# Optimization experiments

Measured on AMD Instinct MI355X. Metric: run time of the kernel, lower is better.

Reference implementation:

```python
import jax, jax.numpy as jnp
import numpy as np

N_HEADS = 16
HEAD_SIZE = 64

def setup_inputs() -> dict:
    key = jax.random.key(0)
    k1, k2 = jax.random.split(key)
    B, N, D = 2, 2048, N_HEADS * HEAD_SIZE
    x = jax.random.normal(k1, (B, N, D), dtype=jnp.float32)
    # lecun_normal-ish scale for the QKV kernel
    W_qkv = jax.random.normal(k2, (D, 3 * D), dtype=jnp.float32) * (1.0 / np.sqrt(D))
    return {"x": x, "W_qkv": W_qkv}

def reference(x, W_qkv):
    B, N, D = x.shape
    H, Dh = N_HEADS, HEAD_SIZE
    qkv = x @ W_qkv                                  # [B,N,3D]
    q, k, v = jnp.split(qkv, 3, axis=-1)
    q = q.reshape(B, N, H, Dh)
    k = k.reshape(B, N, H, Dh)
    v = v.reshape(B, N, H, Dh)
    dist = jnp.einsum('bihd,bjhd->bhij', q, k) / jnp.sqrt(jnp.asarray(Dh, dtype=x.dtype))
    mask = jnp.tril(jnp.ones((N, N), dtype=bool))[None, None, :, :]
    dist = jnp.where(mask, dist, -jnp.inf)
    attn = jax.nn.softmax(dist, axis=-1)             # [B,H,N,N]
    out_heads = jnp.einsum('bhij,bjhd->bihd', attn, v)
    return out_heads.reshape(B, N, H * Dh)
```

## Files before the change

kernel.cpp:

```cpp
#include <hip/hip_runtime.h>

typedef __attribute__((ext_vector_type(8))) short bf16x8;
typedef __attribute__((ext_vector_type(4))) float f32x4;
typedef __attribute__((ext_vector_type(16))) float f32x16;
typedef __attribute__((ext_vector_type(2))) unsigned int u32x2;

#define DEVI static __device__ __forceinline__

namespace {
constexpr int NSEQ = 2048, NH = 16;
constexpr int D = 1024, D3 = 3072;
}

DEVI unsigned short f2bf(float f) {
  union { float f; unsigned int u; } v; v.f = f;
  unsigned int r = v.u + 0x7FFFu + ((v.u >> 16) & 1u);
  return (unsigned short)(r >> 16);
}

DEVI void gload16(const unsigned short* g, unsigned short* lds_) {
  __builtin_amdgcn_global_load_lds(
      (const __attribute__((address_space(1))) unsigned int*)g,
      (__attribute__((address_space(3))) unsigned int*)lds_, 16, 0, 0);
}

DEVI f32x4 mfma16(bf16x8 a, bf16x8 b, f32x4 c) {
  return __builtin_amdgcn_mfma_f32_16x16x32_bf16(a, b, c, 0, 0, 0);
}

DEVI f32x16 mfma32(bf16x8 a, bf16x8 b, f32x16 c) {
  return __builtin_amdgcn_mfma_f32_32x32x16_bf16(a, b, c, 0, 0, 0);
}

DEVI float exp2g(float x) {
#if __has_builtin(__builtin_amdgcn_exp2f)
  return __builtin_amdgcn_exp2f(x);
#else
  return exp2f(x);
#endif
}

DEVI unsigned int cvtpk(float a, float b) {
  unsigned int r;
  asm("v_cvt_pk_bf16_f32 %0, %1, %2" : "=v"(r) : "v"(a), "v"(b));
  return r;
}

DEVI u32x2 pswap2(unsigned int a, unsigned int b) {
  return __builtin_amdgcn_permlane32_swap(a, b, false, false);
}
DEVI float xmax_halves(float v) {
  union { float f; unsigned int u; } c; c.f = v;
  u32x2 r = pswap2(c.u, c.u);
  union { unsigned int u; float f; } x, y; x.u = r.x; y.u = r.y;
  return fmaxf(x.f, y.f);
}

union U4 { unsigned int u[4]; bf16x8 v; };

__global__ __launch_bounds__(256) void prep_k(const float* __restrict__ x,
                                              const float* __restrict__ W,
                                              unsigned short* __restrict__ xb,
                                              unsigned short* __restrict__ Wt) {
  __shared__ float t[32][33];
  const int bid = blockIdx.x;
  if (bid < 4096) {
    int i = (bid * 256 + threadIdx.x) * 4;
    float4 v = *reinterpret_cast<const float4*>(x + i);
    ushort4 o;
    o.x = f2bf(v.x); o.y = f2bf(v.y); o.z = f2bf(v.z); o.w = f2bf(v.w);
    *reinterpret_cast<ushort4*>(xb + i) = o;
  } else {
    const int b2 = bid - 4096;
    const int c0 = (b2 % 96) * 32, k0 = (b2 / 96) * 32;
    const int tx = threadIdx.x & 31, ty = threadIdx.x >> 5;
#pragma unroll
    for (int r = 0; r < 32; r += 8)
      t[ty + r][tx] = W[(size_t)(k0 + ty + r) * D3 + c0 + tx];
    __syncthreads();
#pragma unroll
    for (int r = 0; r < 32; r += 8)
      Wt[(size_t)(c0 + ty + r) * D + k0 + tx] = f2bf(t[tx][ty + r]);
  }
}

__global__ __launch_bounds__(256) void qkv_gemm_k(const unsigned short* __restrict__ xb,
                                                  const unsigned short* __restrict__ Wt,
                                                  unsigned short* __restrict__ qw,
                                                  unsigned short* __restrict__ kw,
                                                  unsigned short* __restrict__ vtw) {
  __shared__ unsigned short smA[128 * 32];
  __shared__ unsigned short smB[128 * 32];
  const int tid = threadIdx.x, w = tid >> 6, l = tid & 63;
  const int m0 = blockIdx.x * 128, n0 = blockIdx.y * 128;
  const int wm = w >> 1, wn = w & 1;

  const unsigned short* ga[2]; const unsigned short* gb[2];
  unsigned short* la[2]; unsigned short* lb[2];
#pragma unroll
  for (int i = 0; i < 2; ++i) {
    int idx = tid + i * 256;
    int row = idx >> 2;
    int blk = (idx & 3) ^ ((row >> 1) & 3);
    ga[i] = xb + (size_t)(m0 + row) * D + blk * 8;
    gb[i] = Wt + (size_t)(n0 + row) * D + blk * 8;
    la[i] = smA + (w * 64 + i * 256) * 8;
    lb[i] = smB + (w * 64 + i * 256) * 8;
  }

  f32x4 acc[4][4];
#pragma unroll
  for (int a = 0; a < 4; ++a)
#pragma unroll
    for (int b = 0; b < 4; ++b) acc[a][b] = (f32x4){0.f, 0.f, 0.f, 0.f};

  for (int kt = 0; kt < D / 32; ++kt) {
    __syncthreads();
#pragma unroll
    for (int i = 0; i < 2; ++i) {
      gload16(ga[i] + kt * 32, la[i]);
      gload16(gb[i] + kt * 32, lb[i]);
    }
    asm volatile("s_waitcnt vmcnt(0)" ::: "memory");
    __syncthreads();

    bf16x8 af[4], bfr[4];
#pragma unroll
    for (int a = 0; a < 4; ++a) {
      int arow = wm * 64 + a * 16 + (l & 15);
      int blk = (l >> 4) ^ ((arow >> 1) & 3);
      af[a] = *reinterpret_cast<const bf16x8*>(smA + arow * 32 + blk * 8);
    }
#pragma unroll
    for (int b = 0; b < 4; ++b) {
      int brow = wn * 64 + b * 16 + (l & 15);
      int blk = (l >> 4) ^ ((brow >> 1) & 3);
      bfr[b] = *reinterpret_cast<const bf16x8*>(smB + brow * 32 + blk * 8);
    }
#pragma unroll
    for (int a = 0; a < 4; ++a)
#pragma unroll
      for (int b = 0; b < 4; ++b)
        acc[a][b] = mfma16(af[a], bfr[b], acc[a][b]);
  }

  const int which = n0 >> 10;
#pragma unroll
  for (int a = 0; a < 4; ++a) {
#pragma unroll
    for (int b = 0; b < 4; ++b) {
#pragma unroll
      for (int r = 0; r < 4; ++r) {
        int grow = m0 + wm * 64 + a * 16 + (l >> 4) * 4 + r;
        int gcol = n0 + wn * 64 + b * 16 + (l & 15);
        float v = acc[a][b][r];
        int bb = grow >> 11, n = grow & 2047;
        int cc = gcol & 1023, h = cc >> 6, dh = cc & 63;
        size_t bh = (size_t)bb * NH + h;
        if (which == 0)
          qw[(bh * NSEQ + n) * 64 + dh] = f2bf(v * 0.18033688011112042f);
        else if (which == 1)
          kw[(bh * NSEQ + n) * 64 + dh] = f2bf(v);
        else
          vtw[(bh * 64 + dh) * NSEQ + n] = f2bf(v);
      }
    }
  }
}

__global__ __launch_bounds__(512, 4) void attn_k(const unsigned short* __restrict__ qw,
                                                 const unsigned short* __restrict__ kw,
                                                 const unsigned short* __restrict__ vtw,
                                                 float* __restrict__ out) {
  __shared__ __align__(16) char lds[67584];
  const int tid = threadIdx.x, w = tid >> 6, l = tid & 63;
  const int hi = l >> 5, ql = l & 31;
  const int qsub = w >> 2, par = w & 3;

  const int wg = blockIdx.x;
  const int xcd = wg & 7, rest = wg >> 3;
  const int bhl = rest >> 4;
  const int j = rest & 15;
  const int bh = xcd * 4 + bhl;
  const int bb = bh >> 4, h = bh & 15;

  const unsigned short* qb = qw + (size_t)bh * NSEQ * 64;
  const unsigned short* kb = kw + (size_t)bh * NSEQ * 64;
  const unsigned short* vb = vtw + (size_t)bh * 64 * NSEQ;

  const int sr = tid >> 3, sc = (tid & 7) ^ (sr & 7);

#define STAGE4(TB)                                                              \
  do {                                                                          \
    _Pragma("unroll")                                                           \
    for (int i_ = 0; i_ < 8; ++i_) {                                            \
      const int T_ = i_ >> 1, kv_ = i_ & 1;                                     \
      const int gt_ = (TB) + T_;                                                \
      if (gt_ <= qt) {                                                          \
        unsigned short* d_ =                                                    \
            (unsigned short*)(lds + T_ * 16384 + kv_ * 8192) + w * 512;         \
        if (kv_ == 0)                                                           \
          gload16(kb + ((size_t)(gt_ * 64 + sr) * 64 + sc * 8), d_);            \
        else                                                                    \
          gload16(vb + ((size_t)sr * NSEQ + gt_ * 64 + sc * 8), d_);            \
      }                                                                         \
    }                                                                           \
  } while (0)

  for (int seg = 0; seg < 2; ++seg) {
    const int qt = seg ? j : (31 - j);
    const int qbase = qt * 64;
    const int qg = qbase + qsub * 32 + ql;

    bf16x8 qf[4];
#pragma unroll
    for (int ds = 0; ds < 4; ++ds)
      qf[ds] = *reinterpret_cast<const bf16x8*>(qb + (size_t)qg * 64 + ds * 16 + hi * 8);

    float m = -1e30f, lsum = 0.f;
    f32x16 O0, O1;
#pragma unroll
    for (int r2 = 0; r2 < 16; ++r2) { O0[r2] = 0.f; O1[r2] = 0.f; }

    const int nsup = (qt >> 2) + 1;
    for (int s = 0; s < nsup; ++s) {
      const int tb = 4 * s;
      __syncthreads();
      STAGE4(tb);
      asm volatile("s_waitcnt vmcnt(0)" ::: "memory");
      __syncthreads();

      const int t = tb + par;
      if (t <= qt) {
        const char* Kb = lds + par * 16384;
        const char* Vb = Kb + 8192;

        f32x16 S0, S1;
#pragma unroll
        for (int r2 = 0; r2 < 16; ++r2) { S0[r2] = 0.f; S1[r2] = 0.f; }
        __builtin_amdgcn_s_setprio(1);
#pragma unroll
        for (int ds = 0; ds < 4; ++ds) {
          bf16x8 k0 = *reinterpret_cast<const bf16x8*>(
              Kb + ql * 128 + (((2 * ds + hi) ^ (ql & 7)) << 4));
          bf16x8 k1 = *reinterpret_cast<const bf16x8*>(
              Kb + (32 + ql) * 128 + (((2 * ds + hi) ^ (ql & 7)) << 4));
          S0 = mfma32(k0, qf[ds], S0);
          S1 = mfma32(k1, qf[ds], S1);
        }
        __builtin_amdgcn_s_setprio(0);

        if (t == qt) {
#pragma unroll
          for (int reg = 0; reg < 16; ++reg) {
            const int krow = (reg & 3) + 8 * (reg >> 2) + 4 * hi;
            if (64 * t + krow > qg) S0[reg] = -1e30f;
            if (64 * t + 32 + krow > qg) S1[reg] = -1e30f;
          }
        }

        float t0 = fmaxf(S0[0], S1[0]), t1 = fmaxf(S0[1], S1[1]);
        float t2 = fmaxf(S0[2], S1[2]), t3 = fmaxf(S0[3], S1[3]);
#pragma unroll
        for (int r2 = 4; r2 < 16; r2 += 4) {
          t0 = fmaxf(t0, fmaxf(S0[r2], S1[r2]));
          t1 = fmaxf(t1, fmaxf(S0[r2 + 1], S1[r2 + 1]));
          t2 = fmaxf(t2, fmaxf(S0[r2 + 2], S1[r2 + 2]));
          t3 = fmaxf(t3, fmaxf(S0[r2 + 3], S1[r2 + 3]));
        }
        float tmax = xmax_halves(fmaxf(fmaxf(t0, t1), fmaxf(t2, t3)));

        if (!__all(tmax <= m + 8.0f)) {
          const float mn = fmaxf(m, tmax);
          const float g = exp2g(m - mn);
          m = mn;
          lsum *= g;
#pragma unroll
          for (int r2 = 0; r2 < 16; ++r2) { O0[r2] *= g; O1[r2] *= g; }
        }

        float rA = 0.f, rB = 0.f, rC = 0.f, rD = 0.f;
#pragma unroll
        for (int r2 = 0; r2 < 16; r2 += 4) {
          S0[r2] = exp2g(S0[r2] - m);         S1[r2] = exp2g(S1[r2] - m);
          S0[r2 + 1] = exp2g(S0[r2 + 1] - m); S1[r2 + 1] = exp2g(S1[r2 + 1] - m);
          S0[r2 + 2] = exp2g(S0[r2 + 2] - m); S1[r2 + 2] = exp2g(S1[r2 + 2] - m);
          S0[r2 + 3] = exp2g(S0[r2 + 3] - m); S1[r2 + 3] = exp2g(S1[r2 + 3] - m);
          rA += S0[r2] + S1[r2];
          rB += S0[r2 + 1] + S1[r2 + 1];
          rC += S0[r2 + 2] + S1[r2 + 2];
          rD += S0[r2 + 3] + S1[r2 + 3];
        }
        {
          float rsum = (rA + rB) + (rC + rD);
          union { float f; unsigned int u; } c; c.f = rsum;
          u32x2 r = pswap2(c.u, c.u);
          union { unsigned int u; float f; } x, y; x.u = r.x; y.u = r.y;
          lsum += x.f + y.f;
        }

        bf16x8 pf[4];
#pragma unroll
        for (int ct = 0; ct < 2; ++ct) {
          unsigned int u[4][2];
#pragma unroll
          for (int c = 0; c < 4; ++c) {
            if (ct == 0) {
              u[c][0] = cvtpk(S0[4 * c], S0[4 * c + 1]);
              u[c][1] = cvtpk(S0[4 * c + 2], S0[4 * c + 3]);
            } else {
              u[c][0] = cvtpk(S1[4 * c], S1[4 * c + 1]);
              u[c][1] = cvtpk(S1[4 * c + 2], S1[4 * c + 3]);
            }
          }
#pragma unroll
          for (int kk = 0; kk < 2; ++kk) {
            u32x2 rw0 = pswap2(u[2 * kk][0], u[2 * kk + 1][0]);
            u32x2 rw1 = pswap2(u[2 * kk][1], u[2 * kk + 1][1]);
            U4 f;
            f.u[0] = rw0.x; f.u[1] = rw1.x;
            f.u[2] = rw0.y; f.u[3] = rw1.y;
            pf[2 * ct + kk] = f.v;
          }
        }

        __builtin_amdgcn_s_setprio(1);
#pragma unroll
        for (int ks = 0; ks < 4; ++ks) {
          bf16x8 v0 = *reinterpret_cast<const bf16x8*>(
              Vb + ql * 128 + (((2 * ks + hi) ^ (ql & 7)) << 4));
          bf16x8 v1 = *reinterpret_cast<const bf16x8*>(
              Vb + (32 + ql) * 128 + (((2 * ks + hi) ^ (ql & 7)) << 4));
          O0 = mfma32(v0, pf[ks], O0);
          O1 = mfma32(v1, pf[ks], O1);
        }
        __builtin_amdgcn_s_setprio(0);
      }
    }

    __syncthreads();
    float* mlp = (float*)(lds + 65536);
    if (l < 32) { mlp[w * 64 + l] = m; mlp[w * 64 + 32 + l] = lsum; }
    __syncthreads();
    {
      float M = m, L = 0.f;
#pragma unroll
      for (int q = 0; q < 4; ++q)
        M = fmaxf(M, mlp[(qsub * 4 + q) * 64 + ql]);
#pragma unroll
      for (int q = 0; q < 4; ++q)
        L += mlp[(qsub * 4 + q) * 64 + 32 + ql] *
             exp2g(mlp[(qsub * 4 + q) * 64 + ql] - M);
      const float phi = exp2g(m - M) / L;
      float* mo = (float*)(lds + w * 8192);
#pragma unroll
      for (int reg = 0; reg < 16; ++reg) {
        const int dr = (reg & 3) + 8 * (reg >> 2) + 4 * hi;
        const int d1 = 32 + dr;
        mo[ql * 64 + (((dr >> 2) ^ (ql & 7)) << 2) + (dr & 3)] = O0[reg] * phi;
        mo[ql * 64 + (((d1 >> 2) ^ (ql & 7)) << 2) + (d1 & 3)] = O1[reg] * phi;
      }
    }
    __syncthreads();
    {
      const int qq = tid >> 3;
      const int dq = (tid & 7) * 8;
      const int qsr = qq >> 5, qrow = qq & 31;
      float* op = out + ((size_t)bb * NSEQ + qbase + qq) * D + h * 64 + dq;
#pragma unroll
      for (int c2 = 0; c2 < 2; ++c2) {
        const int ch = ((dq >> 2) + c2) ^ (qrow & 7);
        float4 s4 = make_float4(0.f, 0.f, 0.f, 0.f);
#pragma unroll
        for (int p = 0; p < 4; ++p) {
          const float* bufp = (const float*)(lds + (qsr * 4 + p) * 8192);
          float4 v = *reinterpret_cast<const float4*>(bufp + qrow * 64 + ch * 4);
          s4.x += v.x; s4.y += v.y; s4.z += v.z; s4.w += v.w;
        }
        *reinterpret_cast<float4*>(op + c2 * 4) = s4;
      }
    }
    __syncthreads();
  }
#undef STAGE4
}

extern "C" void kernel_launch(void* const* d_in, const int* in_sizes, int n_in,
                              void* d_out, int out_size, void* d_ws, size_t ws_size,
                              hipStream_t stream) {
  const float* x = (const float*)d_in[0];
  const float* W = (const float*)d_in[1];
  float* out = (float*)d_out;
  char* ws = (char*)d_ws;
  unsigned short* xb  = (unsigned short*)(ws);
  unsigned short* Wt  = (unsigned short*)(ws + 8388608);
  unsigned short* qw  = (unsigned short*)(ws + 14680064);
  unsigned short* kw  = (unsigned short*)(ws + 23068672);
  unsigned short* vtw = (unsigned short*)(ws + 31457280);

  prep_k<<<7168, 256, 0, stream>>>(x, W, xb, Wt);
  qkv_gemm_k<<<dim3(32, 24), 256, 0, stream>>>(xb, Wt, qw, kw, vtw);
  attn_k<<<512, 512, 0, stream>>>(qw, kw, vtw, out);
}
```

Before: 90.40 us.

## Double-buffer K/V tiles and double attention block size to 128 query rows

```diff
diff --git a/kernel.cpp b/kernel.cpp
--- a/kernel.cpp
+++ b/kernel.cpp
@@ -168,19 +168,19 @@
   }
 }
 
-__global__ __launch_bounds__(512, 4) void attn_k(const unsigned short* __restrict__ qw,
-                                                 const unsigned short* __restrict__ kw,
-                                                 const unsigned short* __restrict__ vtw,
-                                                 float* __restrict__ out) {
-  __shared__ __align__(16) char lds[67584];
+__global__ __launch_bounds__(1024, 4) void attn_k(const unsigned short* __restrict__ qw,
+                                                  const unsigned short* __restrict__ kw,
+                                                  const unsigned short* __restrict__ vtw,
+                                                  float* __restrict__ out) {
+  __shared__ __align__(16) char lds[135168];
   const int tid = threadIdx.x, w = tid >> 6, l = tid & 63;
   const int hi = l >> 5, ql = l & 31;
   const int qsub = w >> 2, par = w & 3;
 
   const int wg = blockIdx.x;
   const int xcd = wg & 7, rest = wg >> 3;
-  const int bhl = rest >> 4;
-  const int j = rest & 15;
+  const int bhl = rest >> 3;
+  const int j = rest & 7;
   const int bh = xcd * 4 + bhl;
   const int bb = bh >> 4, h = bh & 15;
 
@@ -188,18 +188,20 @@
   const unsigned short* kb = kw + (size_t)bh * NSEQ * 64;
   const unsigned short* vb = vtw + (size_t)bh * 64 * NSEQ;
 
-  const int sr = tid >> 3, sc = (tid & 7) ^ (sr & 7);
-
-#define STAGE4(TB)                                                              \
+  const int kvw = (w >> 3) & 1;
+  const int idxl = ((w & 7) << 6) + l;
+  const int sr = idxl >> 3, sc = (idxl & 7) ^ (sr & 7);
+  const int dofs = (w & 7) << 9;
+
+#define STAGE4(SL, TB, MAXT)                                                    \
   do {                                                                          \
     _Pragma("unroll")                                                           \
-    for (int i_ = 0; i_ < 8; ++i_) {                                            \
-      const int T_ = i_ >> 1, kv_ = i_ & 1;                                     \
+    for (int T_ = 0; T_ < 4; ++T_) {                                            \
       const int gt_ = (TB) + T_;                                                \
-      if (gt_ <= qt) {                                                          \
-        unsigned short* d_ =                                                    \
-            (unsigned short*)(lds + T_ * 16384 + kv_ * 8192) + w * 512;         \
-        if (kv_ == 0)                                                           \
+      if (gt_ <= (MAXT)) {                                                      \
+        unsigned short* d_ = (unsigned short*)(lds + (SL) * 65536 +             \
+                                               T_ * 16384 + kvw * 8192) + dofs; \
+        if (kvw == 0)                                                           \
           gload16(kb + ((size_t)(gt_ * 64 + sr) * 64 + sc * 8), d_);            \
         else                                                                    \
           gload16(vb + ((size_t)sr * NSEQ + gt_ * 64 + sc * 8), d_);            \
@@ -208,9 +210,11 @@
   } while (0)
 
   for (int seg = 0; seg < 2; ++seg) {
-    const int qt = seg ? j : (31 - j);
-    const int qbase = qt * 64;
+    const int Qt = seg ? j : (15 - j);
+    const int qbase = Qt * 128;
     const int qg = qbase + qsub * 32 + ql;
+    const int maxt = 2 * Qt + 1;
+    const int dt = 2 * Qt + (qsub >> 1);
 
     bf16x8 qf[4];
 #pragma unroll
@@ -222,17 +226,14 @@
 #pragma unroll
     for (int r2 = 0; r2 < 16; ++r2) { O0[r2] = 0.f; O1[r2] = 0.f; }
 
-    const int nsup = (qt >> 2) + 1;
+    const int nsup = (2 * Qt + 5) >> 2;
+    STAGE4(0, 0, maxt);
     for (int s = 0; s < nsup; ++s) {
-      const int tb = 4 * s;
       __syncthreads();
-      STAGE4(tb);
-      asm volatile("s_waitcnt vmcnt(0)" ::: "memory");
-      __syncthreads();
-
-      const int t = tb + par;
-      if (t <= qt) {
-        const char* Kb = lds + par * 16384;
+      if (s + 1 < nsup) STAGE4((s + 1) & 1, 4 * (s + 1), maxt);
+      const int t = 4 * s + par;
+      if (t <= dt) {
+        const char* Kb = lds + (s & 1) * 65536 + par * 16384;
         const char* Vb = Kb + 8192;
 
         f32x16 S0, S1;
@@ -250,7 +251,7 @@
         }
         __builtin_amdgcn_s_setprio(0);
 
-        if (t == qt) {
+        if (t == dt) {
 #pragma unroll
           for (int reg = 0; reg < 16; ++reg) {
             const int krow = (reg & 3) + 8 * (reg >> 2) + 4 * hi;
@@ -339,7 +340,7 @@
     }
 
     __syncthreads();
-    float* mlp = (float*)(lds + 65536);
+    float* mlp = (float*)(lds + 131072);
     if (l < 32) { mlp[w * 64 + l] = m; mlp[w * 64 + 32 + l] = lsum; }
     __syncthreads();
     {
@@ -400,5 +401,5 @@
 
   prep_k<<<7168, 256, 0, stream>>>(x, W, xb, Wt);
   qkv_gemm_k<<<dim3(32, 24), 256, 0, stream>>>(xb, Wt, qw, kw, vtw);
-  attn_k<<<512, 512, 0, stream>>>(qw, kw, vtw, out);
-}
+  attn_k<<<256, 1024, 0, stream>>>(qw, kw, vtw, out);
+}
```

Result: slower. 96.24 us (+6.5%).

## Give each wave its own query rows and load K/V straight into registers

Applied to the files above, without the earlier changes.

```diff
diff --git a/kernel.cpp b/kernel.cpp
--- a/kernel.cpp
+++ b/kernel.cpp
@@ -168,221 +168,190 @@
   }
 }
 
-__global__ __launch_bounds__(512, 4) void attn_k(const unsigned short* __restrict__ qw,
-                                                 const unsigned short* __restrict__ kw,
-                                                 const unsigned short* __restrict__ vtw,
-                                                 float* __restrict__ out) {
-  __shared__ __align__(16) char lds[67584];
+__global__ __launch_bounds__(256) void attn_k(const unsigned short* __restrict__ qw,
+                                              const unsigned short* __restrict__ kw,
+                                              const unsigned short* __restrict__ vtw,
+                                              float* __restrict__ out) {
+  __shared__ __align__(16) float osm[4][2048];
   const int tid = threadIdx.x, w = tid >> 6, l = tid & 63;
   const int hi = l >> 5, ql = l & 31;
-  const int qsub = w >> 2, par = w & 3;
 
   const int wg = blockIdx.x;
-  const int xcd = wg & 7, rest = wg >> 3;
-  const int bhl = rest >> 4;
-  const int j = rest & 15;
+  const int xcd = wg & 7;
+  const int bhl = (wg >> 3) & 3;
+  const int k16 = wg >> 5;
+  const int i = (k16 < 8) ? (15 - k16) : (k16 - 8);
   const int bh = xcd * 4 + bhl;
   const int bb = bh >> 4, h = bh & 15;
+  const int a = 4 * i + w;
+  const int klen = (a >> 1) + 1;
+  const int q0 = a * 32;
+  const int qg = q0 + ql;
 
   const unsigned short* qb = qw + (size_t)bh * NSEQ * 64;
   const unsigned short* kb = kw + (size_t)bh * NSEQ * 64;
   const unsigned short* vb = vtw + (size_t)bh * 64 * NSEQ;
 
-  const int sr = tid >> 3, sc = (tid & 7) ^ (sr & 7);
-
-#define STAGE4(TB)                                                              \
-  do {                                                                          \
-    _Pragma("unroll")                                                           \
-    for (int i_ = 0; i_ < 8; ++i_) {                                            \
-      const int T_ = i_ >> 1, kv_ = i_ & 1;                                     \
-      const int gt_ = (TB) + T_;                                                \
-      if (gt_ <= qt) {                                                          \
-        unsigned short* d_ =                                                    \
-            (unsigned short*)(lds + T_ * 16384 + kv_ * 8192) + w * 512;         \
-        if (kv_ == 0)                                                           \
-          gload16(kb + ((size_t)(gt_ * 64 + sr) * 64 + sc * 8), d_);            \
-        else                                                                    \
-          gload16(vb + ((size_t)sr * NSEQ + gt_ * 64 + sc * 8), d_);            \
-      }                                                                         \
-    }                                                                           \
+  bf16x8 qf[4];
+#pragma unroll
+  for (int ds = 0; ds < 4; ++ds)
+    qf[ds] = *reinterpret_cast<const bf16x8*>(qb + (size_t)qg * 64 + ds * 16 + hi * 8);
+
+  float m = -1e30f, lsum = 0.f;
+  f32x16 O0, O1;
+#pragma unroll
+  for (int r2 = 0; r2 < 16; ++r2) { O0[r2] = 0.f; O1[r2] = 0.f; }
+
+  bf16x8 kf0[4], kf1[4], vf0[4], vf1[4];
+
+#define LOADK(T_)                                                       \
+  do {                                                                  \
+    const unsigned short* kt_ = kb + (size_t)(T_) * 4096;               \
+    _Pragma("unroll")                                                   \
+    for (int ds_ = 0; ds_ < 4; ++ds_) {                                 \
+      kf0[ds_] = *reinterpret_cast<const bf16x8*>(                      \
+          kt_ + ql * 64 + (2 * ds_ + hi) * 8);                          \
+      kf1[ds_] = *reinterpret_cast<const bf16x8*>(                      \
+          kt_ + (32 + ql) * 64 + (2 * ds_ + hi) * 8);                   \
+    }                                                                   \
   } while (0)
-
-  for (int seg = 0; seg < 2; ++seg) {
-    const int qt = seg ? j : (31 - j);
-    const int qbase = qt * 64;
-    const int qg = qbase + qsub * 32 + ql;
-
-    bf16x8 qf[4];
-#pragma unroll
-    for (int ds = 0; ds < 4; ++ds)
-      qf[ds] = *reinterpret_cast<const bf16x8*>(qb + (size_t)qg * 64 + ds * 16 + hi * 8);
-
-    float m = -1e30f, lsum = 0.f;
-    f32x16 O0, O1;
-#pragma unroll
-    for (int r2 = 0; r2 < 16; ++r2) { O0[r2] = 0.f; O1[r2] = 0.f; }
-
-    const int nsup = (qt >> 2) + 1;
-    for (int s = 0; s < nsup; ++s) {
-      const int tb = 4 * s;
-      __syncthreads();
-      STAGE4(tb);
-      asm volatile("s_waitcnt vmcnt(0)" ::: "memory");
-      __syncthreads();
-
-      const int t = tb + par;
-      if (t <= qt) {
-        const char* Kb = lds + par * 16384;
-        const char* Vb = Kb + 8192;
-
-        f32x16 S0, S1;
-#pragma unroll
-        for (int r2 = 0; r2 < 16; ++r2) { S0[r2] = 0.f; S1[r2] = 0.f; }
-        __builtin_amdgcn_s_setprio(1);
-#pragma unroll
-        for (int ds = 0; ds < 4; ++ds) {
-          bf16x8 k0 = *reinterpret_cast<const bf16x8*>(
-              Kb + ql * 128 + (((2 * ds + hi) ^ (ql & 7)) << 4));
-          bf16x8 k1 = *reinterpret_cast<const bf16x8*>(
-              Kb + (32 + ql) * 128 + (((2 * ds + hi) ^ (ql & 7)) << 4));
-          S0 = mfma32(k0, qf[ds], S0);
-          S1 = mfma32(k1, qf[ds], S1);
+#define LOADV(T_)                                                       \
+  do {                                                                  \
+    const unsigned short* vt_ = vb + (size_t)(T_) * 64;                 \
+    _Pragma("unroll")                                                   \
+    for (int ks_ = 0; ks_ < 4; ++ks_) {                                 \
+      vf0[ks_] = *reinterpret_cast<const bf16x8*>(                      \
+          vt_ + ql * 2048 + (2 * ks_ + hi) * 8);                        \
+      vf1[ks_] = *reinterpret_cast<const bf16x8*>(                      \
+          vt_ + (32 + ql) * 2048 + (2 * ks_ + hi) * 8);                 \
+    }                                                                   \
+  } while (0)
+
+  LOADK(0);
+  LOADV(0);
+  for (int t = 0; t < klen; ++t) {
+    f32x16 S0, S1;
+#pragma unroll
+    for (int r2 = 0; r2 < 16; ++r2) { S0[r2] = 0.f; S1[r2] = 0.f; }
+    __builtin_amdgcn_s_setprio(1);
+#pragma unroll
+    for (int ds = 0; ds < 4; ++ds) {
+      S0 = mfma32(kf0[ds], qf[ds], S0);
+      S1 = mfma32(kf1[ds], qf[ds], S1);
+    }
+    __builtin_amdgcn_s_setprio(0);
+
+    if (t + 1 < klen) LOADK(t + 1);
+
+    if (t == klen - 1) {
+#pragma unroll
+      for (int reg = 0; reg < 16; ++reg) {
+        const int krow = (reg & 3) + 8 * (reg >> 2) + 4 * hi;
+        if (64 * t + krow > qg) S0[reg] = -1e30f;
+        if (64 * t + 32 + krow > qg) S1[reg] = -1e30f;
+      }
+    }
+
+    float t0 = fmaxf(S0[0], S1[0]), t1 = fmaxf(S0[1], S1[1]);
+    float t2 = fmaxf(S0[2], S1[2]), t3 = fmaxf(S0[3], S1[3]);
+#pragma unroll
+    for (int r2 = 4; r2 < 16; r2 += 4) {
+      t0 = fmaxf(t0, fmaxf(S0[r2], S1[r2]));
+      t1 = fmaxf(t1, fmaxf(S0[r2 + 1], S1[r2 + 1]));
+      t2 = fmaxf(t2, fmaxf(S0[r2 + 2], S1[r2 + 2]));
+      t3 = fmaxf(t3, fmaxf(S0[r2 + 3], S1[r2 + 3]));
+    }
+    float tmax = xmax_halves(fmaxf(fmaxf(t0, t1), fmaxf(t2, t3)));
+
+    if (!__all(tmax <= m + 8.0f)) {
+      const float mn = fmaxf(m, tmax);
+      const float g = exp2g(m - mn);
+      m = mn;
+      lsum *= g;
+#pragma unroll
+      for (int r2 = 0; r2 < 16; ++r2) { O0[r2] *= g; O1[r2] *= g; }
+    }
+
+    float rA = 0.f, rB = 0.f, rC = 0.f, rD = 0.f;
+#pragma unroll
+    for (int r2 = 0; r2 < 16; r2 += 4) {
+      S0[r2] = exp2g(S0[r2] - m);         S1[r2] = exp2g(S1[r2] - m);
+      S0[r2 + 1] = exp2g(S0[r2 + 1] - m); S1[r2 + 1] = exp2g(S1[r2 + 1] - m);
+      S0[r2 + 2] = exp2g(S0[r2 + 2] - m); S1[r2 + 2] = exp2g(S1[r2 + 2] - m);
+      S0[r2 + 3] = exp2g(S0[r2 + 3] - m); S1[r2 + 3] = exp2g(S1[r2 + 3] - m);
+      rA += S0[r2] + S1[r2];
+      rB += S0[r2 + 1] + S1[r2 + 1];
+      rC += S0[r2 + 2] + S1[r2 + 2];
+      rD += S0[r2 + 3] + S1[r2 + 3];
+    }
+    {
+      float rsum = (rA + rB) + (rC + rD);
+      union { float f; unsigned int u; } c; c.f = rsum;
+      u32x2 r = pswap2(c.u, c.u);
+      union { unsigned int u; float f; } x, y; x.u = r.x; y.u = r.y;
+      lsum += x.f + y.f;
+    }
+
+    bf16x8 pf[4];
+#pragma unroll
+    for (int ct = 0; ct < 2; ++ct) {
+      unsigned int u[4][2];
+#pragma unroll
+      for (int c = 0; c < 4; ++c) {
+        if (ct == 0) {
+          u[c][0] = cvtpk(S0[4 * c], S0[4 * c + 1]);
+          u[c][1] = cvtpk(S0[4 * c + 2], S0[4 * c + 3]);
+        } else {
+          u[c][0] = cvtpk(S1[4 * c], S1[4 * c + 1]);
+          u[c][1] = cvtpk(S1[4 * c + 2], S1[4 * c + 3]);
         }
-        __builtin_amdgcn_s_setprio(0);
-
-        if (t == qt) {
-#pragma unroll
-          for (int reg = 0; reg < 16; ++reg) {
-            const int krow = (reg & 3) + 8 * (reg >> 2) + 4 * hi;
-            if (64 * t + krow > qg) S0[reg] = -1e30f;
-            if (64 * t + 32 + krow > qg) S1[reg] = -1e30f;
-          }
-        }
-
-        float t0 = fmaxf(S0[0], S1[0]), t1 = fmaxf(S0[1], S1[1]);
-        float t2 = fmaxf(S0[2], S1[2]), t3 = fmaxf(S0[3], S1[3]);
-#pragma unroll
-        for (int r2 = 4; r2 < 16; r2 += 4) {
-          t0 = fmaxf(t0, fmaxf(S0[r2], S1[r2]));
-          t1 = fmaxf(t1, fmaxf(S0[r2 + 1], S1[r2 + 1]));
-          t2 = fmaxf(t2, fmaxf(S0[r2 + 2], S1[r2 + 2]));
-          t3 = fmaxf(t3, fmaxf(S0[r2 + 3], S1[r2 + 3]));
-        }
-        float tmax = xmax_halves(fmaxf(fmaxf(t0, t1), fmaxf(t2, t3)));
-
-        if (!__all(tmax <= m + 8.0f)) {
-          const float mn = fmaxf(m, tmax);
-          const float g = exp2g(m - mn);
-          m = mn;
-          lsum *= g;
-#pragma unroll
-          for (int r2 = 0; r2 < 16; ++r2) { O0[r2] *= g; O1[r2] *= g; }
-        }
-
-        float rA = 0.f, rB = 0.f, rC = 0.f, rD = 0.f;
-#pragma unroll
-        for (int r2 = 0; r2 < 16; r2 += 4) {
-          S0[r2] = exp2g(S0[r2] - m);         S1[r2] = exp2g(S1[r2] - m);
-          S0[r2 + 1] = exp2g(S0[r2 + 1] - m); S1[r2 + 1] = exp2g(S1[r2 + 1] - m);
-          S0[r2 + 2] = exp2g(S0[r2 + 2] - m); S1[r2 + 2] = exp2g(S1[r2 + 2] - m);
-          S0[r2 + 3] = exp2g(S0[r2 + 3] - m); S1[r2 + 3] = exp2g(S1[r2 + 3] - m);
-          rA += S0[r2] + S1[r2];
-          rB += S0[r2 + 1] + S1[r2 + 1];
-          rC += S0[r2 + 2] + S1[r2 + 2];
-          rD += S0[r2 + 3] + S1[r2 + 3];
-        }
-        {
-          float rsum = (rA + rB) + (rC + rD);
-          union { float f; unsigned int u; } c; c.f = rsum;
-          u32x2 r = pswap2(c.u, c.u);
-          union { unsigned int u; float f; } x, y; x.u = r.x; y.u = r.y;
-          lsum += x.f + y.f;
-        }
-
-        bf16x8 pf[4];
-#pragma unroll
-        for (int ct = 0; ct < 2; ++ct) {
-          unsigned int u[4][2];
-#pragma unroll
-          for (int c = 0; c < 4; ++c) {
-            if (ct == 0) {
-              u[c][0] = cvtpk(S0[4 * c], S0[4 * c + 1]);
-              u[c][1] = cvtpk(S0[4 * c + 2], S0[4 * c + 3]);
-            } else {
-              u[c][0] = cvtpk(S1[4 * c], S1[4 * c + 1]);
-              u[c][1] = cvtpk(S1[4 * c + 2], S1[4 * c + 3]);
-            }
-          }
-#pragma unroll
-          for (int kk = 0; kk < 2; ++kk) {
-            u32x2 rw0 = pswap2(u[2 * kk][0], u[2 * kk + 1][0]);
-            u32x2 rw1 = pswap2(u[2 * kk][1], u[2 * kk + 1][1]);
-            U4 f;
-            f.u[0] = rw0.x; f.u[1] = rw1.x;
-            f.u[2] = rw0.y; f.u[3] = rw1.y;
-            pf[2 * ct + kk] = f.v;
-          }
-        }
-
-        __builtin_amdgcn_s_setprio(1);
-#pragma unroll
-        for (int ks = 0; ks < 4; ++ks) {
-          bf16x8 v0 = *reinterpret_cast<const bf16x8*>(
-              Vb + ql * 128 + (((2 * ks + hi) ^ (ql & 7)) << 4));
-          bf16x8 v1 = *reinterpret_cast<const bf16x8*>(
-              Vb + (32 + ql) * 128 + (((2 * ks + hi) ^ (ql & 7)) << 4));
-          O0 = mfma32(v0, pf[ks], O0);
-          O1 = mfma32(v1, pf[ks], O1);
-        }
-        __builtin_amdgcn_s_setprio(0);
       }
-    }
-
-    __syncthreads();
-    float* mlp = (float*)(lds + 65536);
-    if (l < 32) { mlp[w * 64 + l] = m; mlp[w * 64 + 32 + l] = lsum; }
-    __syncthreads();
-    {
-      float M = m, L = 0.f;
-#pragma unroll
-      for (int q = 0; q < 4; ++q)
-        M = fmaxf(M, mlp[(qsub * 4 + q) * 64 + ql]);
-#pragma unroll
-      for (int q = 0; q < 4; ++q)
-        L += mlp[(qsub * 4 + q) * 64 + 32 + ql] *
-             exp2g(mlp[(qsub * 4 + q) * 64 + ql] - M);
-      const float phi = exp2g(m - M) / L;
-      float* mo = (float*)(lds + w * 8192);
-#pragma unroll
-      for (int reg = 0; reg < 16; ++reg) {
-        const int dr = (reg & 3) + 8 * (reg >> 2) + 4 * hi;
-        const int d1 = 32 + dr;
-        mo[ql * 64 + (((dr >> 2) ^ (ql & 7)) << 2) + (dr & 3)] = O0[reg] * phi;
-        mo[ql * 64 + (((d1 >> 2) ^ (ql & 7)) << 2) + (d1 & 3)] = O1[reg] * phi;
+#pragma unroll
+      for (int kk = 0; kk < 2; ++kk) {
+        u32x2 rw0 = pswap2(u[2 * kk][0], u[2 * kk + 1][0]);
+        u32x2 rw1 = pswap2(u[2 * kk][1], u[2 * kk + 1][1]);
+        U4 f;
+        f.u[0] = rw0.x; f.u[1] = rw1.x;
+        f.u[2] = rw0.y; f.u[3] = rw1.y;
+        pf[2 * ct + kk] = f.v;
       }
     }
-    __syncthreads();
-    {
-      const int qq = tid >> 3;
-      const int dq = (tid & 7) * 8;
-      const int qsr = qq >> 5, qrow = qq & 31;
-      float* op = out + ((size_t)bb * NSEQ + qbase + qq) * D + h * 64 + dq;
-#pragma unroll
-      for (int c2 = 0; c2 < 2; ++c2) {
-        const int ch = ((dq >> 2) + c2) ^ (qrow & 7);
-        float4 s4 = make_float4(0.f, 0.f, 0.f, 0.f);
-#pragma unroll
-        for (int p = 0; p < 4; ++p) {
-          const float* bufp = (const float*)(lds + (qsr * 4 + p) * 8192);
-          float4 v = *reinterpret_cast<const float4*>(bufp + qrow * 64 + ch * 4);
-          s4.x += v.x; s4.y += v.y; s4.z += v.z; s4.w += v.w;
-        }
-        *reinterpret_cast<float4*>(op + c2 * 4) = s4;
-      }
-    }
-    __syncthreads();
-  }
-#undef STAGE4
+
+    __builtin_amdgcn_s_setprio(1);
+#pragma unroll
+    for (int ks = 0; ks < 4; ++ks) {
+      O0 = mfma32(vf0[ks], pf[ks], O0);
+      O1 = mfma32(vf1[ks], pf[ks], O1);
+    }
+    __builtin_amdgcn_s_setprio(0);
+
+    if (t + 1 < klen) LOADV(t + 1);
+  }
+#undef LOADK
+#undef LOADV
+
+  const float linv = 1.0f / lsum;
+  float* mo = osm[w];
+#pragma unroll
+  for (int reg = 0; reg < 16; ++reg) {
+    const int dr = (reg & 3) + 8 * (reg >> 2) + 4 * hi;
+    const int d1 = 32 + dr;
+    mo[ql * 64 + (((dr >> 2) ^ (ql & 7)) << 2) + (dr & 3)] = O0[reg] * linv;
+    mo[ql * 64 + (((d1 >> 2) ^ (ql & 7)) << 2) + (d1 & 3)] = O1[reg] * linv;
+  }
+  asm volatile("s_waitcnt lgkmcnt(0)" ::: "memory");
+  __builtin_amdgcn_sched_barrier(0);
+  {
+    const int qrow = l >> 1;
+    const int cb = (l & 1) * 8;
+    float* op = out + ((size_t)bb * NSEQ + q0 + qrow) * D + h * 64 + (l & 1) * 32;
+#pragma unroll
+    for (int c = 0; c < 8; ++c) {
+      const int ch = (cb + c) ^ (qrow & 7);
+      float4 v = *reinterpret_cast<const float4*>(mo + qrow * 64 + ch * 4);
+      *reinterpret_cast<float4*>(op + c * 4) = v;
+    }
+  }
 }
 
 extern "C" void kernel_launch(void* const* d_in, const int* in_sizes, int n_in,
@@ -400,5 +369,5 @@
 
   prep_k<<<7168, 256, 0, stream>>>(x, W, xb, Wt);
   qkv_gemm_k<<<dim3(32, 24), 256, 0, stream>>>(xb, Wt, qw, kw, vtw);
-  attn_k<<<512, 512, 0, stream>>>(qw, kw, vtw, out);
-}
+  attn_k<<<512, 256, 0, stream>>>(qw, kw, vtw, out);
+}
```

New measurement: 114.0 us. +26.1%, slower.
